# Optimization experiments

Measured on AMD Instinct MI355X. Metric: run time of the kernel, lower is better.

## Reference

```python
import jax, jax.numpy as jnp
import numpy as np

N, E, D, H, Dh, B = 100000, 600000, 128, 8, 16, 20
NEG_SLOPE = 0.2  # DGL GATConv default

def setup_inputs() -> dict:
    key = jax.random.key(0)
    ks = jax.random.split(key, 10)
    stdv = 1.0 / np.sqrt(D)
    return {
        "input": jax.random.normal(ks[0], (N, D), jnp.float32),
        "h0": jax.random.normal(ks[1], (N, D), jnp.float32),
        "src": jax.random.randint(ks[2], (E,), 0, N),
        "dst": jax.random.randint(ks[3], (E,), 0, N),
        "cums": jnp.arange(0, N + 1, N // B, dtype=jnp.int32),  # B equal subgraphs
        "l": 2,
        "lamda": jnp.float32(0.5),
        "alpha": jnp.float32(0.1),
        "W_fc": jax.random.normal(ks[4], (D, H * Dh), jnp.float32) * 0.05,
        "attn_l": jax.random.normal(ks[5], (H, Dh), jnp.float32) * 0.05,
        "attn_r": jax.random.normal(ks[6], (H, Dh), jnp.float32) * 0.05,
        "gat_bias": jnp.zeros((H * Dh,), jnp.float32),
        "W_comb": jax.random.uniform(ks[7], (2 * D, D), jnp.float32, -stdv, stdv),
        "gamma": jnp.ones((1, D), jnp.float32),
        "beta": jnp.zeros((1, D), jnp.float32),
    }

def reference(input, h0, src, dst, cums, l, lamda, alpha, W_fc, attn_l, attn_r,
              gat_bias, W_comb, gamma, beta):
    n = input.shape[0]
    # --- DGL GATConv: fc -> per-edge scores -> edge softmax by dst -> scatter ---
    h = (input @ W_fc).reshape(n, H, Dh)                    # (N,H,Dh)
    el = (h * attn_l).sum(-1)                               # (N,H)
    er = (h * attn_r).sum(-1)                               # (N,H)
    e = jax.nn.leaky_relu(el[src] + er[dst], NEG_SLOPE)     # (E,H)
    m = jax.ops.segment_max(e, dst, num_segments=n)         # (N,H)
    ex = jnp.exp(e - m[dst])
    denom = jax.ops.segment_sum(ex, dst, num_segments=n)
    a = ex / denom[dst]                                     # (E,H)
    msg = a[:, :, None] * h[src]                            # (E,H,Dh)
    rst = jax.ops.segment_sum(msg, dst, num_segments=n)
    x = (rst + gat_bias.reshape(1, H, Dh)).reshape(n, H * Dh)
    # --- GCNII combine ---
    theta = jnp.minimum(1.0, jnp.log(lamda / l + 1.0))
    support = jnp.concatenate([x, h0], axis=1)              # (N,2D)
    r = (1.0 - alpha) * x + alpha * h0
    x = theta * (support @ W_comb) + (1.0 - theta) * r
    x = x + input
    # --- per-subgraph GraphNorm (unbiased std, like torch.std) ---
    sid = jnp.searchsorted(cums, jnp.arange(n), side="right") - 1  # (N,)
    nb = cums.shape[0] - 1
    cnt = jax.ops.segment_sum(jnp.ones((n,), x.dtype), sid, num_segments=nb)
    mean = jax.ops.segment_sum(x, sid, num_segments=nb) / cnt[:, None]
    c = x - mean[sid]
    var = jax.ops.segment_sum(c * c, sid, num_segments=nb) / (cnt - 1.0)[:, None]
    std = jnp.sqrt(var)
    return gamma * (c / (std[sid] + 1e-5)) + beta
```

## Files before the change

kernel.cpp:

```cpp
#include <hip/hip_runtime.h>
#include <hip/hip_bf16.h>

#define NEG_SLOPE 0.2f
#define STATS_SPLIT 50

typedef short bf16x8 __attribute__((ext_vector_type(8)));
typedef float f32x4 __attribute__((ext_vector_type(4)));

__device__ __forceinline__ unsigned short f2bf(float f) {
    unsigned int u = __float_as_uint(f);
    unsigned int r = (u + 0x7fffu + ((u >> 16) & 1u)) >> 16;
    return (unsigned short)r;
}
__device__ __forceinline__ float bf2f(unsigned short h) {
    return __uint_as_float(((unsigned int)h) << 16);
}

__global__ __launch_bounds__(256) void prep_kernel(
    const float* __restrict__ W_fc, const float* __restrict__ attn_l,
    const float* __restrict__ attn_r, const float* __restrict__ W_comb,
    const int* __restrict__ l_p, const float* __restrict__ lamda_p,
    const float* __restrict__ alpha_p,
    unsigned short* __restrict__ Wt_fc, unsigned short* __restrict__ Wt_cb)
{
    const float alpha = alpha_p[0];
    const float theta = fminf(1.0f, logf(lamda_p[0] / (float)l_p[0] + 1.0f));
    const float c1 = (1.f - theta) * (1.f - alpha);
    const float c2 = (1.f - theta) * alpha;

    const int t = blockIdx.x * 256 + threadIdx.x;
    const int stride = gridDim.x * 256;
    for (int i = t; i < 128 * 128; i += stride) {
        const int c = i >> 7, k = i & 127;
        Wt_fc[c * 128 + k] = f2bf(W_fc[k * 128 + c]);
    }
    for (int i = t; i < 8 * 128; i += stride) {
        const int hd = i >> 7, k = i & 127;
        float sl = 0.f, sr = 0.f;
        for (int d = 0; d < 16; ++d) {
            const float w = W_fc[k * 128 + hd * 16 + d];
            sl += w * attn_l[hd * 16 + d];
            sr += w * attn_r[hd * 16 + d];
        }
        Wt_fc[(128 + hd) * 128 + k] = f2bf(sl);
        Wt_fc[(136 + hd) * 128 + k] = f2bf(sr);
    }
    for (int i = t; i < 128 * 256; i += stride) {
        const int c = i >> 8, k = i & 255;
        float w = theta * W_comb[k * 128 + c];
        if (k == c) w += c1;
        if (k == c + 128) w += c2;
        Wt_cb[c * 256 + k] = f2bf(w);
    }
}

__global__ __launch_bounds__(256) void fc_gemm_kernel(
    const float* __restrict__ A, const unsigned short* __restrict__ Wt,
    unsigned short* __restrict__ h, float* __restrict__ el,
    float* __restrict__ er, int n)
{
    __shared__ unsigned short As[64][36];
    __shared__ unsigned short Bs[144][36];
    const int tid = threadIdx.x;
    const int wave = tid >> 6;
    const int lane = tid & 63;
    const int m16 = lane & 15;
    const int kg = lane >> 4;
    const int rowBase = blockIdx.x * 64;

    f32x4 acc[9];
#pragma unroll
    for (int t = 0; t < 9; ++t) acc[t] = (f32x4){0.f, 0.f, 0.f, 0.f};

    const int rS = tid >> 2;
    const int pS = tid & 3;

    for (int ci = 0; ci < 4; ++ci) {
        const int kc = ci * 32;
        if (ci) __syncthreads();
        {
            int row = rowBase + rS;
            if (row >= n) row = n - 1;
            const float4 v0 = *(const float4*)&A[(long long)row * 128 + kc + pS * 8];
            const float4 v1 = *(const float4*)&A[(long long)row * 128 + kc + pS * 8 + 4];
            bf16x8 pk;
            pk[0] = (short)f2bf(v0.x); pk[1] = (short)f2bf(v0.y);
            pk[2] = (short)f2bf(v0.z); pk[3] = (short)f2bf(v0.w);
            pk[4] = (short)f2bf(v1.x); pk[5] = (short)f2bf(v1.y);
            pk[6] = (short)f2bf(v1.z); pk[7] = (short)f2bf(v1.w);
            *(bf16x8*)&As[rS][pS * 8] = pk;
        }
        for (int i = tid; i < 576; i += 256) {
            const int r = i >> 2, p = i & 3;
            *(bf16x8*)&Bs[r][p * 8] =
                *(const bf16x8*)&Wt[r * 128 + kc + p * 8];
        }
        __syncthreads();

        const bf16x8 afrag = *(const bf16x8*)&As[wave * 16 + m16][kg * 8];
#pragma unroll
        for (int t = 0; t < 9; ++t) {
            const bf16x8 bfrag = *(const bf16x8*)&Bs[t * 16 + m16][kg * 8];
            acc[t] = __builtin_amdgcn_mfma_f32_16x16x32_bf16(afrag, bfrag, acc[t], 0, 0, 0);
        }
    }

    const int r0 = rowBase + wave * 16 + kg * 4;
#pragma unroll
    for (int t = 0; t < 8; ++t) {
#pragma unroll
        for (int j = 0; j < 4; ++j) {
            const int row = r0 + j;
            if (row < n)
                h[(long long)row * 128 + t * 16 + m16] = f2bf(acc[t][j]);
        }
    }
#pragma unroll
    for (int j = 0; j < 4; ++j) {
        const int row = r0 + j;
        if (row < n) {
            const float v = acc[8][j];
            if (m16 < 8) el[(long long)row * 8 + m16] = v;
            else         er[(long long)row * 8 + (m16 - 8)] = v;
        }
    }
}

__global__ __launch_bounds__(256) void hist_kernel(
    const int* __restrict__ dst, int* __restrict__ deg, int E)
{
    const int i = blockIdx.x * 256 + threadIdx.x;
    if (i < E) atomicAdd(&deg[dst[i]], 1);
}

__global__ __launch_bounds__(256) void scan1_kernel(
    const int* __restrict__ deg, int* __restrict__ row,
    int* __restrict__ blockSums, int n)
{
    __shared__ int sdata[256];
    const int t = threadIdx.x;
    const int base = blockIdx.x * 1024 + t * 4;
    int v[4];
    int tot = 0;
#pragma unroll
    for (int j = 0; j < 4; ++j) {
        v[j] = (base + j < n) ? deg[base + j] : 0;
        tot += v[j];
    }
    sdata[t] = tot;
    __syncthreads();
    for (int off = 1; off < 256; off <<= 1) {
        const int x = (t >= off) ? sdata[t - off] : 0;
        __syncthreads();
        sdata[t] += x;
        __syncthreads();
    }
    if (t == 255) blockSums[blockIdx.x] = sdata[255];
    int run = sdata[t] - tot;
#pragma unroll
    for (int j = 0; j < 4; ++j) {
        if (base + j < n) row[base + j] = run;
        run += v[j];
    }
}

__global__ __launch_bounds__(128) void scan2_kernel(
    int* __restrict__ blockSums, int nb)
{
    __shared__ int sdata[128];
    const int t = threadIdx.x;
    const int v = (t < nb) ? blockSums[t] : 0;
    sdata[t] = v;
    __syncthreads();
    for (int off = 1; off < 128; off <<= 1) {
        const int x = (t >= off) ? sdata[t - off] : 0;
        __syncthreads();
        sdata[t] += x;
        __syncthreads();
    }
    if (t < nb) blockSums[t] = sdata[t] - v;
}

__global__ __launch_bounds__(256) void scan3_kernel(
    int* __restrict__ row, int* __restrict__ cursor,
    const int* __restrict__ blockSums, int n, int E)
{
    const int i = blockIdx.x * 256 + threadIdx.x;
    if (i == 0) row[n] = E;
    if (i >= n) return;
    const int r = row[i] + blockSums[i >> 10];
    row[i] = r;
    cursor[i] = r;
}

__global__ __launch_bounds__(256) void scatter_kernel(
    const int* __restrict__ src, const int* __restrict__ dst,
    int* __restrict__ cursor, int* __restrict__ srcs, int E)
{
    const int i = blockIdx.x * 256 + threadIdx.x;
    if (i >= E) return;
    const int pos = atomicAdd(&cursor[dst[i]], 1);
    srcs[pos] = src[i];
}

__global__ __launch_bounds__(256) void aggregate_kernel(
    const float* __restrict__ el, const float* __restrict__ er,
    const unsigned short* __restrict__ h, const int* __restrict__ row,
    const int* __restrict__ srcs, float* __restrict__ rst, int n)
{
    const int wave = blockIdx.x * 4 + (threadIdx.x >> 6);
    const int lane = threadIdx.x & 63;
    if (wave >= n) return;
    const int d = wave;
    const int start = row[d], end = row[d + 1];
    const int hd0 = lane >> 4;
    const float er0 = er[(long long)d * 8 + hd0];
    const float er1 = er[(long long)d * 8 + hd0 + 4];

    float acc0 = 0.f, acc1 = 0.f, den0 = 0.f, den1 = 0.f;
    for (int p = start; p < end; ++p) {
        const int s = srcs[p];
        float e0 = el[(long long)s * 8 + hd0] + er0;
        float e1 = el[(long long)s * 8 + hd0 + 4] + er1;
        e0 = e0 >= 0.f ? e0 : NEG_SLOPE * e0;
        e1 = e1 >= 0.f ? e1 : NEG_SLOPE * e1;
        const float w0 = __expf(e0);
        const float w1 = __expf(e1);
        den0 += w0; den1 += w1;
        acc0 += w0 * bf2f(h[(long long)s * 128 + lane]);
        acc1 += w1 * bf2f(h[(long long)s * 128 + 64 + lane]);
    }
    const float r0 = (end > start) ? acc0 / den0 : 0.f;
    const float r1 = (end > start) ? acc1 / den1 : 0.f;
    rst[(long long)d * 128 + lane] = r0;
    rst[(long long)d * 128 + 64 + lane] = r1;
}

__global__ __launch_bounds__(256) void combine_gemm_kernel(
    const float* __restrict__ rst, const float* __restrict__ gat_bias,
    const float* __restrict__ h0, const float* __restrict__ input,
    const unsigned short* __restrict__ Wt,
    float* __restrict__ x, int n)
{
    __shared__ unsigned short As[2][64][36];
    __shared__ unsigned short Bs[2][128][36];
    const int tid = threadIdx.x;
    const int wave = tid >> 6;
    const int lane = tid & 63;
    const int m16 = lane & 15;
    const int kg = lane >> 4;
    const int rowBase = blockIdx.x * 64;

    f32x4 acc[8];
#pragma unroll
    for (int t = 0; t < 8; ++t) acc[t] = (f32x4){0.f, 0.f, 0.f, 0.f};

    const int rS = tid >> 2;
    const int pS = tid & 3;
    const int rB = tid >> 1;
    const int p0 = (tid & 1) * 2;

    float4 va0, va1;
    bf16x8 vb0, vb1;
    int arow = rowBase + rS;
    if (arow >= n) arow = n - 1;
    const long long aoff = (long long)arow * 128;

#define CB_LOAD(ci)                                                           \
    {                                                                         \
        const int kc = (ci) * 32;                                             \
        const int koff = kc & 127;                                            \
        if ((ci) < 4) {                                                       \
            va0 = *(const float4*)&rst[aoff + koff + pS * 8];                 \
            va1 = *(const float4*)&rst[aoff + koff + pS * 8 + 4];             \
            const float4 b0 = *(const float4*)&gat_bias[koff + pS * 8];       \
            const float4 b1 = *(const float4*)&gat_bias[koff + pS * 8 + 4];   \
            va0.x += b0.x; va0.y += b0.y; va0.z += b0.z; va0.w += b0.w;       \
            va1.x += b1.x; va1.y += b1.y; va1.z += b1.z; va1.w += b1.w;       \
        } else {                                                              \
            va0 = *(const float4*)&h0[aoff + koff + pS * 8];                  \
            va1 = *(const float4*)&h0[aoff + koff + pS * 8 + 4];              \
        }                                                                     \
        vb0 = *(const bf16x8*)&Wt[rB * 256 + kc + p0 * 8];                    \
        vb1 = *(const bf16x8*)&Wt[rB * 256 + kc + p0 * 8 + 8];                \
    }

#define CB_WRITE(buf)                                                         \
    {                                                                         \
        bf16x8 pk;                                                            \
        pk[0] = (short)f2bf(va0.x); pk[1] = (short)f2bf(va0.y);               \
        pk[2] = (short)f2bf(va0.z); pk[3] = (short)f2bf(va0.w);               \
        pk[4] = (short)f2bf(va1.x); pk[5] = (short)f2bf(va1.y);               \
        pk[6] = (short)f2bf(va1.z); pk[7] = (short)f2bf(va1.w);               \
        *(bf16x8*)&As[buf][rS][pS * 8] = pk;                                  \
        *(bf16x8*)&Bs[buf][rB][p0 * 8] = vb0;                                 \
        *(bf16x8*)&Bs[buf][rB][p0 * 8 + 8] = vb1;                             \
    }

    CB_LOAD(0)
    CB_WRITE(0)
    __syncthreads();

#pragma unroll
    for (int ci = 0; ci < 8; ++ci) {
        const int cur = ci & 1;
        if (ci < 7) CB_LOAD(ci + 1)
        const bf16x8 afrag = *(const bf16x8*)&As[cur][wave * 16 + m16][kg * 8];
#pragma unroll
        for (int t = 0; t < 8; ++t) {
            const bf16x8 bfrag = *(const bf16x8*)&Bs[cur][t * 16 + m16][kg * 8];
            acc[t] = __builtin_amdgcn_mfma_f32_16x16x32_bf16(afrag, bfrag, acc[t], 0, 0, 0);
        }
        if (ci < 7) {
            CB_WRITE(cur ^ 1)
            __syncthreads();
        }
    }
#undef CB_LOAD
#undef CB_WRITE

    const int r0 = rowBase + wave * 16 + kg * 4;
#pragma unroll
    for (int t = 0; t < 8; ++t) {
        const int col = t * 16 + m16;
#pragma unroll
        for (int j = 0; j < 4; ++j) {
            const int row = r0 + j;
            if (row < n) {
                const long long off = (long long)row * 128 + col;
                x[off] = acc[t][j] + input[off];
            }
        }
    }
}

__global__ __launch_bounds__(128) void stats_kernel(
    const float* __restrict__ x, const int* __restrict__ cums,
    float* __restrict__ sums, float* __restrict__ sumsq)
{
    const int b = blockIdx.x / STATS_SPLIT;
    const int part = blockIdx.x % STATS_SPLIT;
    const int tid = threadIdx.x;
    const int start = cums[b], end = cums[b + 1];
    float s = 0.f, s2 = 0.f;
    for (int node = start + part; node < end; node += STATS_SPLIT) {
        const float v = x[(long long)node * 128 + tid];
        s += v;
        s2 += v * v;
    }
    atomicAdd(&sums[b * 128 + tid], s);
    atomicAdd(&sumsq[b * 128 + tid], s2);
}

__global__ __launch_bounds__(128) void finalize_stats_kernel(
    const int* __restrict__ cums, float* __restrict__ sums,
    float* __restrict__ sumsq)
{
    const int b = blockIdx.x;
    const int tid = threadIdx.x;
    const float cnt = (float)(cums[b + 1] - cums[b]);
    const float s = sums[b * 128 + tid];
    const float s2 = sumsq[b * 128 + tid];
    const float mean = s / cnt;
    float var = (s2 - s * mean) / (cnt - 1.f);
    var = fmaxf(var, 0.f);
    sums[b * 128 + tid] = mean;
    sumsq[b * 128 + tid] = 1.f / (sqrtf(var) + 1e-5f);
}

__global__ __launch_bounds__(256) void norm_kernel(
    const float* __restrict__ x, const float* __restrict__ mean,
    const float* __restrict__ istd, const int* __restrict__ cums, int nb,
    const float* __restrict__ gamma, const float* __restrict__ beta,
    float* __restrict__ out, int n)
{
    const long long gid = (long long)blockIdx.x * 256 + threadIdx.x;
    const int node = (int)(gid >> 5);
    if (node >= n) return;
    const int f4 = (int)(gid & 31);
    int lo = 0, hi = nb;
    while (hi - lo > 1) {
        const int mid = (lo + hi) >> 1;
        if (cums[mid] <= node) lo = mid; else hi = mid;
    }
    const float4 m = *(const float4*)&mean[lo * 128 + f4 * 4];
    const float4 is = *(const float4*)&istd[lo * 128 + f4 * 4];
    const float4 g = *(const float4*)&gamma[f4 * 4];
    const float4 bt = *(const float4*)&beta[f4 * 4];
    const float4 v = *(const float4*)&x[(long long)node * 128 + f4 * 4];
    float4 o;
    o.x = g.x * ((v.x - m.x) * is.x) + bt.x;
    o.y = g.y * ((v.y - m.y) * is.y) + bt.y;
    o.z = g.z * ((v.z - m.z) * is.z) + bt.z;
    o.w = g.w * ((v.w - m.w) * is.w) + bt.w;
    *(float4*)&out[(long long)node * 128 + f4 * 4] = o;
}

extern "C" void kernel_launch(void* const* d_in, const int* in_sizes, int n_in,
                              void* d_out, int out_size, void* d_ws, size_t ws_size,
                              hipStream_t stream) {
    const float* input   = (const float*)d_in[0];
    const float* h0      = (const float*)d_in[1];
    const int*   src     = (const int*)d_in[2];
    const int*   dst     = (const int*)d_in[3];
    const int*   cums    = (const int*)d_in[4];
    const int*   l_p     = (const int*)d_in[5];
    const float* lamda_p = (const float*)d_in[6];
    const float* alpha_p = (const float*)d_in[7];
    const float* W_fc    = (const float*)d_in[8];
    const float* attn_l  = (const float*)d_in[9];
    const float* attn_r  = (const float*)d_in[10];
    const float* gat_bias= (const float*)d_in[11];
    const float* W_comb  = (const float*)d_in[12];
    const float* gamma   = (const float*)d_in[13];
    const float* beta    = (const float*)d_in[14];

    const int n  = in_sizes[0] / 128;
    const int E  = in_sizes[2];
    const int nb = in_sizes[4] - 1;
    float* out = (float*)d_out;

    char* ws = (char*)d_ws;
    size_t o = 0;
#define ALLOC(ptr, type, count)                                              \
    type* ptr = (type*)(ws + o); o = (o + (size_t)(count) * sizeof(type) + 15) & ~(size_t)15;
    ALLOC(h,        unsigned short, (size_t)n * 128)
    ALLOC(el,       float,          (size_t)n * 8)
    ALLOC(er,       float,          (size_t)n * 8)
    ALLOC(rst,      float,          (size_t)n * 128)
    ALLOC(sums,     float,          (size_t)nb * 128)
    ALLOC(sumsq,    float,          (size_t)nb * 128)
    ALLOC(deg,      int,            (size_t)n)
    ALLOC(row_ptr,  int,            (size_t)n + 1)
    ALLOC(cursor,   int,            (size_t)n)
    ALLOC(blockSums,int,            128)
    ALLOC(srcs,     int,            (size_t)E)
    ALLOC(Wt_fc,    unsigned short, 144 * 128)
    ALLOC(Wt_cb,    unsigned short, 128 * 256)
#undef ALLOC

    hipMemsetAsync(deg, 0, (size_t)n * 4, stream);
    hipMemsetAsync(sums, 0, (size_t)nb * 128 * 4, stream);
    hipMemsetAsync(sumsq, 0, (size_t)nb * 128 * 4, stream);

    prep_kernel<<<64, 256, 0, stream>>>(
        W_fc, attn_l, attn_r, W_comb, l_p, lamda_p, alpha_p, Wt_fc, Wt_cb);

    hist_kernel<<<(E + 255) / 256, 256, 0, stream>>>(dst, deg, E);
    const int nblk1 = (n + 1023) / 1024;
    scan1_kernel<<<nblk1, 256, 0, stream>>>(deg, row_ptr, blockSums, n);
    scan2_kernel<<<1, 128, 0, stream>>>(blockSums, nblk1);
    scan3_kernel<<<(n + 255) / 256, 256, 0, stream>>>(row_ptr, cursor, blockSums, n, E);
    scatter_kernel<<<(E + 255) / 256, 256, 0, stream>>>(src, dst, cursor, srcs, E);

    const int gemm_grid = (n + 63) / 64;
    fc_gemm_kernel<<<gemm_grid, 256, 0, stream>>>(input, Wt_fc, h, el, er, n);

    aggregate_kernel<<<(n + 3) / 4, 256, 0, stream>>>(
        el, er, h, row_ptr, srcs, rst, n);

    combine_gemm_kernel<<<gemm_grid, 256, 0, stream>>>(
        rst, gat_bias, h0, input, Wt_cb, out, n);

    stats_kernel<<<nb * STATS_SPLIT, 128, 0, stream>>>(out, cums, sums, sumsq);
    finalize_stats_kernel<<<nb, 128, 0, stream>>>(cums, sums, sumsq);

    const long long norm_threads = (long long)n * 32;
    norm_kernel<<<(int)((norm_threads + 255) / 256), 256, 0, stream>>>(
        out, sums, sumsq, cums, nb, gamma, beta, out, n);
}
```

Before: 270.4 us.

## Store aggregate output as bf16, fold GAT bias into combine epilogue, batch source loads

```diff
diff --git a/kernel.cpp b/kernel.cpp
--- a/kernel.cpp
+++ b/kernel.cpp
@@ -19,9 +19,11 @@
 __global__ __launch_bounds__(256) void prep_kernel(
     const float* __restrict__ W_fc, const float* __restrict__ attn_l,
     const float* __restrict__ attn_r, const float* __restrict__ W_comb,
+    const float* __restrict__ gat_bias,
     const int* __restrict__ l_p, const float* __restrict__ lamda_p,
     const float* __restrict__ alpha_p,
-    unsigned short* __restrict__ Wt_fc, unsigned short* __restrict__ Wt_cb)
+    unsigned short* __restrict__ Wt_fc, unsigned short* __restrict__ Wt_cb,
+    float* __restrict__ bvec)
 {
     const float alpha = alpha_p[0];
     const float theta = fminf(1.0f, logf(lamda_p[0] / (float)l_p[0] + 1.0f));
@@ -51,6 +53,12 @@
         if (k == c) w += c1;
         if (k == c + 128) w += c2;
         Wt_cb[c * 256 + k] = f2bf(w);
+    }
+    for (int c = t; c < 128; c += stride) {
+        float s = c1 * gat_bias[c];
+        for (int k = 0; k < 128; ++k)
+            s += theta * gat_bias[k] * W_comb[k * 128 + c];
+        bvec[c] = s;
     }
 }
 
@@ -206,41 +214,63 @@
 __global__ __launch_bounds__(256) void aggregate_kernel(
     const float* __restrict__ el, const float* __restrict__ er,
     const unsigned short* __restrict__ h, const int* __restrict__ row,
-    const int* __restrict__ srcs, float* __restrict__ rst, int n)
-{
-    const int wave = blockIdx.x * 4 + (threadIdx.x >> 6);
+    const int* __restrict__ srcs, unsigned short* __restrict__ rst, int n)
+{
+    const int d = blockIdx.x * 4 + (threadIdx.x >> 6);
     const int lane = threadIdx.x & 63;
-    if (wave >= n) return;
-    const int d = wave;
+    if (d >= n) return;
     const int start = row[d], end = row[d + 1];
-    const int hd0 = lane >> 4;
-    const float er0 = er[(long long)d * 8 + hd0];
-    const float er1 = er[(long long)d * 8 + hd0 + 4];
-
-    float acc0 = 0.f, acc1 = 0.f, den0 = 0.f, den1 = 0.f;
-    for (int p = start; p < end; ++p) {
-        const int s = srcs[p];
-        float e0 = el[(long long)s * 8 + hd0] + er0;
-        float e1 = el[(long long)s * 8 + hd0 + 4] + er1;
-        e0 = e0 >= 0.f ? e0 : NEG_SLOPE * e0;
-        e1 = e1 >= 0.f ? e1 : NEG_SLOPE * e1;
-        const float w0 = __expf(e0);
-        const float w1 = __expf(e1);
-        den0 += w0; den1 += w1;
-        acc0 += w0 * bf2f(h[(long long)s * 128 + lane]);
-        acc1 += w1 * bf2f(h[(long long)s * 128 + 64 + lane]);
-    }
-    const float r0 = (end > start) ? acc0 / den0 : 0.f;
-    const float r1 = (end > start) ? acc1 / den1 : 0.f;
-    rst[(long long)d * 128 + lane] = r0;
-    rst[(long long)d * 128 + 64 + lane] = r1;
+    const int hd = lane >> 3;
+    const float erd = er[(long long)d * 8 + hd];
+
+    float acc0 = 0.f, acc1 = 0.f, den = 0.f;
+    for (int p = start; p < end; p += 64) {
+        const int cnt = min(64, end - p);
+        const int sv = srcs[p + (lane < cnt ? lane : cnt - 1)];
+        int j = 0;
+        for (; j + 1 < cnt; j += 2) {
+            const int s0 = __shfl(sv, j);
+            const int s1 = __shfl(sv, j + 1);
+            const float g0 = el[(long long)s0 * 8 + hd];
+            const float g1 = el[(long long)s1 * 8 + hd];
+            const unsigned int u0 = *(const unsigned int*)&h[(long long)s0 * 128 + lane * 2];
+            const unsigned int u1 = *(const unsigned int*)&h[(long long)s1 * 128 + lane * 2];
+            float e0 = g0 + erd; e0 = e0 >= 0.f ? e0 : NEG_SLOPE * e0;
+            float e1 = g1 + erd; e1 = e1 >= 0.f ? e1 : NEG_SLOPE * e1;
+            const float w0 = __expf(e0);
+            const float w1 = __expf(e1);
+            den += w0 + w1;
+            acc0 += w0 * __uint_as_float(u0 << 16)
+                  + w1 * __uint_as_float(u1 << 16);
+            acc1 += w0 * __uint_as_float(u0 & 0xffff0000u)
+                  + w1 * __uint_as_float(u1 & 0xffff0000u);
+        }
+        if (j < cnt) {
+            const int s0 = __shfl(sv, j);
+            const unsigned int u0 = *(const unsigned int*)&h[(long long)s0 * 128 + lane * 2];
+            float e0 = el[(long long)s0 * 8 + hd] + erd;
+            e0 = e0 >= 0.f ? e0 : NEG_SLOPE * e0;
+            const float w0 = __expf(e0);
+            den += w0;
+            acc0 += w0 * __uint_as_float(u0 << 16);
+            acc1 += w0 * __uint_as_float(u0 & 0xffff0000u);
+        }
+    }
+    ushort2 o;
+    if (end > start) {
+        const float inv = 1.f / den;
+        o.x = f2bf(acc0 * inv);
+        o.y = f2bf(acc1 * inv);
+    } else {
+        o.x = 0; o.y = 0;
+    }
+    *(ushort2*)&rst[(long long)d * 128 + lane * 2] = o;
 }
 
 __global__ __launch_bounds__(256) void combine_gemm_kernel(
-    const float* __restrict__ rst, const float* __restrict__ gat_bias,
-    const float* __restrict__ h0, const float* __restrict__ input,
-    const unsigned short* __restrict__ Wt,
-    float* __restrict__ x, int n)
+    const unsigned short* __restrict__ rst, const float* __restrict__ h0,
+    const float* __restrict__ input, const unsigned short* __restrict__ Wt,
+    const float* __restrict__ bvec, float* __restrict__ x, int n)
 {
     __shared__ unsigned short As[2][64][36];
     __shared__ unsigned short Bs[2][128][36];
@@ -261,7 +291,7 @@
     const int p0 = (tid & 1) * 2;
 
     float4 va0, va1;
-    bf16x8 vb0, vb1;
+    bf16x8 vr, vb0, vb1;
     int arow = rowBase + rS;
     if (arow >= n) arow = n - 1;
     const long long aoff = (long long)arow * 128;
@@ -271,12 +301,7 @@
         const int kc = (ci) * 32;                                             \
         const int koff = kc & 127;                                            \
         if ((ci) < 4) {                                                       \
-            va0 = *(const float4*)&rst[aoff + koff + pS * 8];                 \
-            va1 = *(const float4*)&rst[aoff + koff + pS * 8 + 4];             \
-            const float4 b0 = *(const float4*)&gat_bias[koff + pS * 8];       \
-            const float4 b1 = *(const float4*)&gat_bias[koff + pS * 8 + 4];   \
-            va0.x += b0.x; va0.y += b0.y; va0.z += b0.z; va0.w += b0.w;       \
-            va1.x += b1.x; va1.y += b1.y; va1.z += b1.z; va1.w += b1.w;       \
+            vr = *(const bf16x8*)&rst[aoff + koff + pS * 8];                  \
         } else {                                                              \
             va0 = *(const float4*)&h0[aoff + koff + pS * 8];                  \
             va1 = *(const float4*)&h0[aoff + koff + pS * 8 + 4];              \
@@ -285,20 +310,24 @@
         vb1 = *(const bf16x8*)&Wt[rB * 256 + kc + p0 * 8 + 8];                \
     }
 
-#define CB_WRITE(buf)                                                         \
+#define CB_WRITE(buf, ci)                                                     \
     {                                                                         \
-        bf16x8 pk;                                                            \
-        pk[0] = (short)f2bf(va0.x); pk[1] = (short)f2bf(va0.y);               \
-        pk[2] = (short)f2bf(va0.z); pk[3] = (short)f2bf(va0.w);               \
-        pk[4] = (short)f2bf(va1.x); pk[5] = (short)f2bf(va1.y);               \
-        pk[6] = (short)f2bf(va1.z); pk[7] = (short)f2bf(va1.w);               \
-        *(bf16x8*)&As[buf][rS][pS * 8] = pk;                                  \
+        if ((ci) < 4) {                                                       \
+            *(bf16x8*)&As[buf][rS][pS * 8] = vr;                              \
+        } else {                                                              \
+            bf16x8 pk;                                                        \
+            pk[0] = (short)f2bf(va0.x); pk[1] = (short)f2bf(va0.y);           \
+            pk[2] = (short)f2bf(va0.z); pk[3] = (short)f2bf(va0.w);           \
+            pk[4] = (short)f2bf(va1.x); pk[5] = (short)f2bf(va1.y);           \
+            pk[6] = (short)f2bf(va1.z); pk[7] = (short)f2bf(va1.w);           \
+            *(bf16x8*)&As[buf][rS][pS * 8] = pk;                              \
+        }                                                                     \
         *(bf16x8*)&Bs[buf][rB][p0 * 8] = vb0;                                 \
         *(bf16x8*)&Bs[buf][rB][p0 * 8 + 8] = vb1;                             \
     }
 
     CB_LOAD(0)
-    CB_WRITE(0)
+    CB_WRITE(0, 0)
     __syncthreads();
 
 #pragma unroll
@@ -312,7 +341,7 @@
             acc[t] = __builtin_amdgcn_mfma_f32_16x16x32_bf16(afrag, bfrag, acc[t], 0, 0, 0);
         }
         if (ci < 7) {
-            CB_WRITE(cur ^ 1)
+            CB_WRITE(cur ^ 1, ci + 1)
             __syncthreads();
         }
     }
@@ -323,12 +352,13 @@
 #pragma unroll
     for (int t = 0; t < 8; ++t) {
         const int col = t * 16 + m16;
+        const float bv = bvec[col];
 #pragma unroll
         for (int j = 0; j < 4; ++j) {
             const int row = r0 + j;
             if (row < n) {
                 const long long off = (long long)row * 128 + col;
-                x[off] = acc[t][j] + input[off];
+                x[off] = acc[t][j] + bv + input[off];
             }
         }
     }
@@ -427,7 +457,7 @@
     ALLOC(h,        unsigned short, (size_t)n * 128)
     ALLOC(el,       float,          (size_t)n * 8)
     ALLOC(er,       float,          (size_t)n * 8)
-    ALLOC(rst,      float,          (size_t)n * 128)
+    ALLOC(rst,      unsigned short, (size_t)n * 128)
     ALLOC(sums,     float,          (size_t)nb * 128)
     ALLOC(sumsq,    float,          (size_t)nb * 128)
     ALLOC(deg,      int,            (size_t)n)
@@ -437,6 +467,7 @@
     ALLOC(srcs,     int,            (size_t)E)
     ALLOC(Wt_fc,    unsigned short, 144 * 128)
     ALLOC(Wt_cb,    unsigned short, 128 * 256)
+    ALLOC(bvec,     float,          128)
 #undef ALLOC
 
     hipMemsetAsync(deg, 0, (size_t)n * 4, stream);
@@ -444,7 +475,8 @@
     hipMemsetAsync(sumsq, 0, (size_t)nb * 128 * 4, stream);
 
     prep_kernel<<<64, 256, 0, stream>>>(
-        W_fc, attn_l, attn_r, W_comb, l_p, lamda_p, alpha_p, Wt_fc, Wt_cb);
+        W_fc, attn_l, attn_r, W_comb, gat_bias, l_p, lamda_p, alpha_p,
+        Wt_fc, Wt_cb, bvec);
 
     hist_kernel<<<(E + 255) / 256, 256, 0, stream>>>(dst, deg, E);
     const int nblk1 = (n + 1023) / 1024;
@@ -460,7 +492,7 @@
         el, er, h, row_ptr, srcs, rst, n);
 
     combine_gemm_kernel<<<gemm_grid, 256, 0, stream>>>(
-        rst, gat_bias, h0, input, Wt_cb, out, n);
+        rst, h0, input, Wt_cb, bvec, out, n);
 
     stats_kernel<<<nb * STATS_SPLIT, 128, 0, stream>>>(out, cums, sums, sumsq);
     finalize_stats_kernel<<<nb, 128, 0, stream>>>(cums, sums, sumsq);
```

After: 246.5 us. 8.8% less time.
